# Kernel optimization log

Measured on AMD Instinct MI355X. Metric: run time of the kernel, lower is better.

The kernel has to match this reference:

```python
import jax, jax.numpy as jnp
import numpy as np

# SS2D (VMamba-style): CrossScan (4 directional traversals) -> per-direction
# input-dependent SSM params -> selective scan recurrence -> CrossMerge -> ChanLayerNorm.

B_SZ, D_IN, H_SZ, W_SZ = 8, 192, 64, 64   # d_inner = ssm_ratio * d_model = 2*96
N_ST, R_DT, K_GRP = 16, 6, 4               # d_state, dt_rank=ceil(96/16), 4 scan dirs
LN_EPS = 1e-5


def setup_inputs() -> dict:
    key = jax.random.key(0)
    ks = jax.random.split(key, 6)
    x = jax.random.normal(ks[0], (B_SZ, D_IN, H_SZ, W_SZ), dtype=jnp.float32)
    x_proj_weight = jax.random.normal(ks[1], (K_GRP, R_DT + 2 * N_ST, D_IN), dtype=jnp.float32) * 0.02
    dt_projs_weight = jax.random.normal(ks[2], (K_GRP, D_IN, R_DT), dtype=jnp.float32) * (R_DT ** -0.5)
    dt_projs_bias = jax.random.normal(ks[3], (K_GRP, D_IN), dtype=jnp.float32) * 0.1
    # A_log init: log(1..N) repeated per channel (mamba v0 init)
    A_logs = jnp.log(jnp.tile(jnp.arange(1, N_ST + 1, dtype=jnp.float32), (K_GRP * D_IN, 1)))
    Ds = jnp.ones((K_GRP * D_IN,), dtype=jnp.float32)
    ln_g = jnp.ones((1, D_IN, 1, 1), dtype=jnp.float32)
    ln_b = jnp.zeros((1, D_IN, 1, 1), dtype=jnp.float32)
    return dict(x=x, x_proj_weight=x_proj_weight, dt_projs_weight=dt_projs_weight,
                dt_projs_bias=dt_projs_bias, A_logs=A_logs, Ds=Ds, ln_g=ln_g, ln_b=ln_b)


def _ss2d(x, x_proj_weight, dt_projs_weight, dt_projs_bias, A_logs, Ds, ln_g, ln_b):
    B, D, H, W = x.shape
    L = H * W
    K = x_proj_weight.shape[0]
    N = A_logs.shape[1]
    R = dt_projs_weight.shape[2]

    # ---- CrossScan: 4 directional flattenings -> xs [B,K,D,L] ----
    x0 = x.reshape(B, D, L)                         # row-major
    x1 = x.transpose(0, 1, 3, 2).reshape(B, D, L)   # column-major (transpose H,W)
    xs = jnp.stack([x0, x1, x0[..., ::-1], x1[..., ::-1]], axis=1)

    # ---- input-dependent SSM params ----
    x_dbl = jnp.einsum('bkdl,kcd->bkcl', xs, x_proj_weight)      # [B,K,R+2N,L]
    dts, Bs, Cs = jnp.split(x_dbl, [R, R + N], axis=2)           # [B,K,R,L],[B,K,N,L],[B,K,N,L]
    dts = jnp.einsum('bkrl,kdr->bkdl', dts, dt_projs_weight)     # [B,K,D,L]
    A = -jnp.exp(A_logs.astype(jnp.float32)).reshape(K, D, N)    # [K,D,N]
    delta = jax.nn.softplus(dts + dt_projs_bias[None, :, :, None])  # [B,K,D,L]

    # ---- selective scan: h_t = exp(delta*A)*h_{t-1} + delta*B_t*u_t; y_t = C_t.h_t ----
    def step(h, inp):
        u_t, d_t, B_t, C_t = inp                     # [B,K,D],[B,K,D],[B,K,N],[B,K,N]
        h = jnp.exp(d_t[..., None] * A) * h + (d_t * u_t)[..., None] * B_t[:, :, None, :]
        y = jnp.einsum('bkdn,bkn->bkd', h, C_t)
        return h, y

    h0 = jnp.zeros((B, K, D, N), dtype=jnp.float32)
    seq = (xs.transpose(3, 0, 1, 2), delta.transpose(3, 0, 1, 2),
           Bs.transpose(3, 0, 1, 2), Cs.transpose(3, 0, 1, 2))
    _, ys = jax.lax.scan(step, h0, seq)              # [L,B,K,D]
    ys = ys.transpose(1, 2, 3, 0) + Ds.reshape(K, D)[None, :, :, None] * xs  # [B,K,D,L]

    # ---- CrossMerge: undo flips/transpose and sum the 4 directions ----
    ym = ys[:, 0:2] + ys[:, 2:4][..., ::-1]          # [B,2,D,L]
    y = ym[:, 0] + ym[:, 1].reshape(B, D, W, H).transpose(0, 1, 3, 2).reshape(B, D, L)
    y = y.reshape(B, D, H, W)

    # ---- ChanLayerNorm over channel dim (biased var) ----
    mean = jnp.mean(y, axis=1, keepdims=True)
    var = jnp.var(y, axis=1, keepdims=True)
    return (y - mean) / jnp.sqrt(var + LN_EPS) * ln_g + ln_b


def reference(x, x_proj_weight, dt_projs_weight, dt_projs_bias, A_logs, Ds, ln_g, ln_b):
    return _ss2d(x, x_proj_weight, dt_projs_weight, dt_projs_bias, A_logs, Ds, ln_g, ln_b)
```

## Files before the change

kernel.cpp:

```cpp
#include <hip/hip_runtime.h>
#include <cstdint>
#include <cstddef>


#define L2E 1.4426950408889634f
#define LN2 0.6931471805599453f
#define NCH 64
#define CHL 64

typedef float f32x2 __attribute__((ext_vector_type(2)));
typedef float f32x4 __attribute__((ext_vector_type(4)));

static __device__ __forceinline__ float fast_rcp(float x) {
#if defined(__has_builtin)
#if __has_builtin(__builtin_amdgcn_rcpf)
  return __builtin_amdgcn_rcpf(x);
#else
  return 1.f / x;
#endif
#else
  return 1.f / x;
#endif
}

static __device__ __forceinline__ f32x2 pk_mul_vv(f32x2 a, f32x2 b) {
  f32x2 d; asm("v_pk_mul_f32 %0, %1, %2" : "=v"(d) : "v"(a), "v"(b)); return d;
}
static __device__ __forceinline__ f32x2 pk_mul_bh(f32x2 a, f32x2 b) {
  f32x2 d;
  asm("v_pk_mul_f32 %0, %1, %2 op_sel:[0,1] op_sel_hi:[1,1]" : "=v"(d) : "v"(a), "v"(b));
  return d;
}
static __device__ __forceinline__ f32x2 pk_mul_sv(f32x2 s, f32x2 v) {
  f32x2 d; asm("v_pk_mul_f32 %0, %1, %2" : "=v"(d) : "s"(s), "v"(v)); return d;
}
static __device__ __forceinline__ f32x2 pk_mul_vs(f32x2 v, f32x2 s) {
  f32x2 d; asm("v_pk_mul_f32 %0, %1, %2" : "=v"(d) : "v"(v), "s"(s)); return d;
}
static __device__ __forceinline__ void pk_h(f32x2& h, f32x2 a, f32x2 t) {
  asm("v_pk_fma_f32 %0, %1, %0, %2" : "+v"(h) : "v"(a), "v"(t));
}
static __device__ __forceinline__ void pk_y(f32x2& y, f32x2 h, f32x2 cs) {
  asm("v_pk_fma_f32 %0, %1, %2, %0" : "+v"(y) : "v"(h), "s"(cs));
}

__global__ __launch_bounds__(256) void k0_xpose(const float* __restrict__ x,
                                                float* __restrict__ xP) {
  __shared__ float t[64 * 193];
  int b = blockIdx.x >> 6, p0 = (blockIdx.x & 63) << 6;
  for (int i = threadIdx.x; i < 64 * 192; i += 256) {
    int d = i >> 6, p = i & 63;
    t[p * 193 + d] = x[((size_t)(b * 192 + d)) * 4096 + p0 + p];
  }
  __syncthreads();
  float* dst = xP + ((size_t)b * 4096 + p0) * 192;
  for (int i = threadIdx.x; i < 64 * 192; i += 256) {
    int p = i / 192, d = i - p * 192;
    dst[i] = t[p * 193 + d];
  }
}

__global__ __launch_bounds__(256) void k1_proj(const float* __restrict__ x,
                                               const float* __restrict__ xpw,
                                               float* __restrict__ proj) {
  __shared__ float W[38 * 192];
  int bid = blockIdx.x;
  int t = bid & 15, k = (bid >> 4) & 3, b = bid >> 6;
  {
    const float4* src = (const float4*)(xpw + k * 38 * 192);
    float4* dst = (float4*)W;
    for (int i = threadIdx.x; i < 38 * 192 / 4; i += 256) dst[i] = src[i];
  }
  __syncthreads();

  int p = (t << 8) + threadIdx.x;
  const float* xb = x + (size_t)b * 192 * 4096 + p;
  float acc[38];
#pragma unroll
  for (int c = 0; c < 38; ++c) acc[c] = 0.f;

  for (int d0 = 0; d0 < 192; d0 += 8) {
    float xr[8];
#pragma unroll
    for (int j = 0; j < 8; ++j) xr[j] = xb[(size_t)(d0 + j) * 4096];
#pragma unroll
    for (int c = 0; c < 38; ++c) {
      const float* wr = &W[c * 192 + d0];
      float4 w0 = *(const float4*)wr;
      float4 w1 = *(const float4*)(wr + 4);
      float a0 = fmaf(w0.x, xr[0], fmaf(w0.y, xr[1], fmaf(w0.z, xr[2], w0.w * xr[3])));
      float a1 = fmaf(w1.x, xr[4], fmaf(w1.y, xr[5], fmaf(w1.z, xr[6], w1.w * xr[7])));
      acc[c] += a0 + a1;
    }
  }

  int hh = p >> 6, ww = p & 63;
  int lp = (k == 0) ? p
         : (k == 1) ? ((ww << 6) | hh)
         : (k == 2) ? (4095 - p)
                    : (4095 - ((ww << 6) | hh));
  float* row = proj + (((size_t)(b * 4 + k)) * 4096 + (size_t)lp) * 40;
#pragma unroll
  for (int q4 = 0; q4 < 9; ++q4) {
    float4 v; v.x = acc[q4 * 4]; v.y = acc[q4 * 4 + 1];
    v.z = acc[q4 * 4 + 2]; v.w = acc[q4 * 4 + 3];
    ((float4*)row)[q4] = v;
  }
  { float4 v; v.x = acc[36]; v.y = acc[37]; v.z = 0.f; v.w = 0.f; ((float4*)row)[9] = v; }
}

struct Pref { f32x4 b[10]; float u; };

static __device__ __forceinline__ void scan_step(const Pref& P, float bias,
                                                 const float w_[6], float Dk,
                                                 f32x2 h2[8], float& r, float* yp) {
  float dts = bias;
  dts = fmaf(w_[0], P.b[0].x, dts);
  dts = fmaf(w_[1], P.b[0].y, dts);
  dts = fmaf(w_[2], P.b[0].z, dts);
  dts = fmaf(w_[3], P.b[0].w, dts);
  dts = fmaf(w_[4], P.b[1].x, dts);
  dts = fmaf(w_[5], P.b[1].y, dts);
  float e1 = __builtin_exp2f(dts * L2E) + 1.f;
  float q = fast_rcp(e1);
  float delta = __builtin_log2f(e1) * LN2;
  float du = delta * P.u;
  r *= q;
  f32x2 a0; a0.x = q; a0.y = q * q;
  f32x2 a1 = pk_mul_bh(a0, a0);
  f32x2 a3 = pk_mul_bh(a1, a1);
  f32x2 a2 = pk_mul_bh(a0, a1);
  f32x2 a4 = pk_mul_bh(a0, a3);
  f32x2 a5 = pk_mul_bh(a1, a3);
  f32x2 a6 = pk_mul_bh(a2, a3);
  f32x2 a7 = pk_mul_bh(a3, a3);
  f32x2 du2; du2.x = du; du2.y = du;
  pk_h(h2[0], a0, pk_mul_sv(P.b[1].zw, du2));
  pk_h(h2[1], a1, pk_mul_sv(P.b[2].xy, du2));
  f32x2 ya = pk_mul_vs(h2[0], P.b[5].zw);
  f32x2 yb = pk_mul_vs(h2[1], P.b[6].xy);
  pk_h(h2[2], a2, pk_mul_sv(P.b[2].zw, du2));
  pk_y(ya, h2[2], P.b[6].zw);
  pk_h(h2[3], a3, pk_mul_sv(P.b[3].xy, du2));
  pk_y(yb, h2[3], P.b[7].xy);
  pk_h(h2[4], a4, pk_mul_sv(P.b[3].zw, du2));
  pk_y(ya, h2[4], P.b[7].zw);
  pk_h(h2[5], a5, pk_mul_sv(P.b[4].xy, du2));
  pk_y(yb, h2[5], P.b[8].xy);
  pk_h(h2[6], a6, pk_mul_sv(P.b[4].zw, du2));
  pk_y(ya, h2[6], P.b[8].zw);
  pk_h(h2[7], a7, pk_mul_sv(P.b[5].xy, du2));
  pk_y(yb, h2[7], P.b[9].xy);
  f32x2 yt = ya + yb;
  *yp = fmaf(Dk, P.u, yt.x + yt.y);
}

__global__ __launch_bounds__(192) void k2a_scan(const float* __restrict__ xP,
                                                const float* __restrict__ proj,
                                                const float* __restrict__ dtw,
                                                const float* __restrict__ dtb,
                                                const float* __restrict__ Ds,
                                                float* __restrict__ ys,
                                                float* __restrict__ hout,
                                                float* __restrict__ Rc) {
  int wg = blockIdx.x;
  int c = wg & (NCH - 1), bk = wg >> 6;
  int k = bk & 3, b = bk >> 2;
  int d = threadIdx.x;

  float w_[6];
  {
    const float* wrow = dtw + (size_t)(k * 192 + d) * 6;
#pragma unroll
    for (int r = 0; r < 6; ++r) w_[r] = wrow[r];
  }
  float bias = dtb[k * 192 + d];
  float Dk = (k == 0) ? (Ds[d] + Ds[192 + d] + Ds[384 + d] + Ds[576 + d]) : 0.f;

  int l0 = c * CHL;
  int p0s  = (k == 0) ? l0 : (k == 1) ? c : (k == 2) ? (4095 - l0) : (4095 - c);
  int pstr = (k == 0) ? 1  : (k == 1) ? 64 : (k == 2) ? -1 : -64;
  ptrdiff_t pinc = (ptrdiff_t)pstr * 192;

  const float* up = xP + ((size_t)b * 4096 + (size_t)p0s) * 192 + d;
  float* yp = ys + (((size_t)(k * 8 + b)) * 4096 + (size_t)p0s) * 192 + d;
  const float* pr = proj + ((size_t)bk * 4096 + l0) * 40;

  f32x2 h2[8];
#pragma unroll
  for (int j = 0; j < 8; ++j) { h2[j].x = 0.f; h2[j].y = 0.f; }
  float r = 1.f;

  Pref A, Bp;
#pragma unroll
  for (int i = 0; i < 10; ++i) A.b[i] = ((const f32x4*)pr)[i];
  A.u = *up;
  pr += 40; up += pinc;

  for (int t = 0; t < CHL - 2; t += 2) {
#pragma unroll
    for (int i = 0; i < 10; ++i) Bp.b[i] = ((const f32x4*)pr)[i];
    Bp.u = *up; pr += 40; up += pinc;
    scan_step(A, bias, w_, Dk, h2, r, yp); yp += pinc;
#pragma unroll
    for (int i = 0; i < 10; ++i) A.b[i] = ((const f32x4*)pr)[i];
    A.u = *up; pr += 40; up += pinc;
    scan_step(Bp, bias, w_, Dk, h2, r, yp); yp += pinc;
  }
#pragma unroll
  for (int i = 0; i < 10; ++i) Bp.b[i] = ((const f32x4*)pr)[i];
  Bp.u = *up;
  scan_step(A, bias, w_, Dk, h2, r, yp); yp += pinc;
  scan_step(Bp, bias, w_, Dk, h2, r, yp);

  float* hst = hout + (((size_t)bk * NCH + c) * 16) * 192 + d;
#pragma unroll
  for (int j = 0; j < 8; ++j) {
    hst[(size_t)(2 * j) * 192]     = h2[j].x;
    hst[(size_t)(2 * j + 1) * 192] = h2[j].y;
  }
  Rc[((size_t)bk * NCH + c) * 192 + d] = r;
}

__global__ __launch_bounds__(192) void k2b_pfx(float* __restrict__ hout,
                                               const float* __restrict__ Rc) {
  int bk = blockIdx.x >> 4, n = blockIdx.x & 15;
  int d = threadIdx.x;
  int e = n + 1;
  float H = 0.f;
  for (int c0 = 0; c0 < NCH; c0 += 4) {
    float hl[4], R[4];
#pragma unroll
    for (int j = 0; j < 4; ++j) {
      size_t cb = (size_t)bk * NCH + c0 + j;
      hl[j] = hout[(cb * 16 + n) * 192 + d];
      R[j] = Rc[cb * 192 + d];
    }
#pragma unroll
    for (int j = 0; j < 4; ++j) {
      size_t cb = (size_t)bk * NCH + c0 + j;
      hout[(cb * 16 + n) * 192 + d] = H;
      float R1 = R[j], R2 = R1 * R1, R4 = R2 * R2, R8 = R4 * R4;
      float Rp = 1.f;
      if (e & 1) Rp *= R1;
      if (e & 2) Rp *= R2;
      if (e & 4) Rp *= R4;
      if (e & 8) Rp *= R8;
      H = fmaf(Rp, H, hl[j]);
    }
  }
}

__global__ __launch_bounds__(192) void k2c_fix(const float* __restrict__ proj,
                                               const float* __restrict__ dtw,
                                               const float* __restrict__ dtb,
                                               const float* __restrict__ hout,
                                               float* __restrict__ ys) {
  int wg = blockIdx.x;
  int c = wg & (NCH - 1), bk = wg >> 6;
  if (c == 0) return;
  int k = bk & 3, b = bk >> 2;
  int d = threadIdx.x;

  float w_[6];
  {
    const float* wrow = dtw + (size_t)(k * 192 + d) * 6;
#pragma unroll
    for (int r = 0; r < 6; ++r) w_[r] = wrow[r];
  }
  float bias = dtb[k * 192 + d];

  f32x2 H2[8];
  {
    const float* hr = hout + (((size_t)bk * NCH + c) * 16) * 192 + d;
#pragma unroll
    for (int j = 0; j < 8; ++j) {
      H2[j].x = hr[(size_t)(2 * j) * 192];
      H2[j].y = hr[(size_t)(2 * j + 1) * 192];
    }
  }

  int l0 = c * CHL;
  int p0s  = (k == 0) ? l0 : (k == 1) ? c : (k == 2) ? (4095 - l0) : (4095 - c);
  int pstr = (k == 0) ? 1  : (k == 1) ? 64 : (k == 2) ? -1 : -64;
  ptrdiff_t pinc = (ptrdiff_t)pstr * 192;

  const float* pr = proj + ((size_t)bk * 4096 + l0) * 40;
  float* yp = ys + (((size_t)(k * 8 + b)) * 4096 + (size_t)p0s) * 192 + d;
  float r = 1.f;

  for (int t = 0; t < CHL; ++t) {
    f32x4 v0 = *(const f32x4*)pr;
    f32x2 v1 = *(const f32x2*)(pr + 4);
    f32x2 c0 = *(const f32x2*)(pr + 22);
    f32x2 c1 = *(const f32x2*)(pr + 24);
    f32x2 c2 = *(const f32x2*)(pr + 26);
    f32x2 c3 = *(const f32x2*)(pr + 28);
    f32x2 c4 = *(const f32x2*)(pr + 30);
    f32x2 c5 = *(const f32x2*)(pr + 32);
    f32x2 c6 = *(const f32x2*)(pr + 34);
    f32x2 c7 = *(const f32x2*)(pr + 36);

    float dts = bias;
    dts = fmaf(w_[0], v0.x, dts);
    dts = fmaf(w_[1], v0.y, dts);
    dts = fmaf(w_[2], v0.z, dts);
    dts = fmaf(w_[3], v0.w, dts);
    dts = fmaf(w_[4], v1.x, dts);
    dts = fmaf(w_[5], v1.y, dts);
    float e1 = __builtin_exp2f(dts * L2E) + 1.f;
    float q = fast_rcp(e1);
    r *= q;
    if (__all(r < 1e-8f)) break;
    f32x2 p0; p0.x = r; p0.y = r * r;
    f32x2 rp1 = pk_mul_bh(p0, p0);
    f32x2 rp3 = pk_mul_bh(rp1, rp1);
    f32x2 rp2 = pk_mul_bh(p0, rp1);
    f32x2 rp4 = pk_mul_bh(p0, rp3);
    f32x2 rp5 = pk_mul_bh(rp1, rp3);
    f32x2 rp6 = pk_mul_bh(rp2, rp3);
    f32x2 rp7 = pk_mul_bh(rp3, rp3);
    f32x2 ya = pk_mul_vs(pk_mul_vv(H2[0], p0),  c0);
    f32x2 yb = pk_mul_vs(pk_mul_vv(H2[1], rp1), c1);
    pk_y(ya, pk_mul_vv(H2[2], rp2), c2);
    pk_y(yb, pk_mul_vv(H2[3], rp3), c3);
    pk_y(ya, pk_mul_vv(H2[4], rp4), c4);
    pk_y(yb, pk_mul_vv(H2[5], rp5), c5);
    pk_y(ya, pk_mul_vv(H2[6], rp6), c6);
    pk_y(yb, pk_mul_vv(H2[7], rp7), c7);
    f32x2 yt = ya + yb;
    *yp += yt.x + yt.y;
    pr += 40; yp += pinc;
  }
}

__global__ __launch_bounds__(256) void k3_ln(const float* __restrict__ ys,
                                             const float* __restrict__ g,
                                             const float* __restrict__ bta,
                                             float* __restrict__ out) {
  __shared__ float tile[64 * 193];
  __shared__ float ps[4][64], pq[4][64];
  __shared__ float mstat[64], rstat[64];
  int b = blockIdx.x >> 6, p0 = (blockIdx.x & 63) << 6;
  const float* s0 = ys + ((size_t)(0 * 8 + b) * 4096 + p0) * 192;
  const float* s1 = ys + ((size_t)(1 * 8 + b) * 4096 + p0) * 192;
  const float* s2 = ys + ((size_t)(2 * 8 + b) * 4096 + p0) * 192;
  const float* s3 = ys + ((size_t)(3 * 8 + b) * 4096 + p0) * 192;
  for (int i = threadIdx.x; i < 64 * 192; i += 256) {
    int p = i / 192, dd = i - p * 192;
    tile[p * 193 + dd] = (s0[i] + s1[i]) + (s2[i] + s3[i]);
  }
  __syncthreads();
  {
    int p = threadIdx.x & 63, qd = threadIdx.x >> 6;
    float s = 0.f, s2a = 0.f;
#pragma unroll
    for (int j = 0; j < 48; ++j) {
      float v = tile[p * 193 + qd * 48 + j];
      s += v; s2a = fmaf(v, v, s2a);
    }
    ps[qd][p] = s; pq[qd][p] = s2a;
  }
  __syncthreads();
  if (threadIdx.x < 64) {
    int p = threadIdx.x;
    float S = ps[0][p] + ps[1][p] + ps[2][p] + ps[3][p];
    float Q = pq[0][p] + pq[1][p] + pq[2][p] + pq[3][p];
    float mu = S * (1.f / 192.f);
    float var = Q * (1.f / 192.f) - mu * mu;
    mstat[p] = mu;
    rstat[p] = rsqrtf(var + 1e-5f);
  }
  __syncthreads();
  for (int i = threadIdx.x; i < 64 * 192; i += 256) {
    int dd = i >> 6, p = i & 63;
    float v = (tile[p * 193 + dd] - mstat[p]) * rstat[p] * g[dd] + bta[dd];
    out[((size_t)(b * 192 + dd)) * 4096 + p0 + p] = v;
  }
}

extern "C" void kernel_launch(void* const* d_in, const int* in_sizes, int n_in,
                              void* d_out, int out_size, void* d_ws, size_t ws_size,
                              hipStream_t stream) {
  const float* x   = (const float*)d_in[0];
  const float* xpw = (const float*)d_in[1];
  const float* dtw = (const float*)d_in[2];
  const float* dtb = (const float*)d_in[3];
  const float* Ds  = (const float*)d_in[5];
  const float* g   = (const float*)d_in[6];
  const float* bta = (const float*)d_in[7];
  float* out = (float*)d_out;

  char* ws = (char*)d_ws;
  float* xP   = (float*)(ws);
  float* proj = (float*)(ws + 25165824);
  float* ys   = (float*)(ws + 46137344);
  float* hout = (float*)(ws + 146800640);
  float* Rc   = (float*)(ws + 171966464);

  k0_xpose<<<512, 256, 0, stream>>>(x, xP);
  k1_proj<<<512, 256, 0, stream>>>(x, xpw, proj);
  k2a_scan<<<2048, 192, 0, stream>>>(xP, proj, dtw, dtb, Ds, ys, hout, Rc);
  k2b_pfx<<<512, 192, 0, stream>>>(hout, Rc);
  k2c_fix<<<2048, 192, 0, stream>>>(proj, dtw, dtb, hout, ys);
  k3_ln<<<512, 256, 0, stream>>>(ys, g, bta, out);
}
```

Baseline: 200.7 us.

## Fuse transpose into projection kernel and loosen fix-up early-exit threshold

Drops the separate k0_xpose kernel. The k=0 blocks of k1_proj now write the channel-last copy xP from the values they already load, which saves one launch and one full read of x. The xP writes are 192-float strided per thread rather than coalesced. In k2c_fix the dt dot product is split into independent partial sums for more ILP, and the C coefficients move from SGPR operands to VGPR operands. The early-exit threshold on the decay product rises from 1e-8 to 2e-5, which skips more correction steps at some cost in accuracy.

```diff
diff --git a/kernel.cpp b/kernel.cpp
--- a/kernel.cpp
+++ b/kernel.cpp
@@ -43,26 +43,14 @@
 static __device__ __forceinline__ void pk_y(f32x2& y, f32x2 h, f32x2 cs) {
   asm("v_pk_fma_f32 %0, %1, %2, %0" : "+v"(y) : "v"(h), "s"(cs));
 }
-
-__global__ __launch_bounds__(256) void k0_xpose(const float* __restrict__ x,
-                                                float* __restrict__ xP) {
-  __shared__ float t[64 * 193];
-  int b = blockIdx.x >> 6, p0 = (blockIdx.x & 63) << 6;
-  for (int i = threadIdx.x; i < 64 * 192; i += 256) {
-    int d = i >> 6, p = i & 63;
-    t[p * 193 + d] = x[((size_t)(b * 192 + d)) * 4096 + p0 + p];
-  }
-  __syncthreads();
-  float* dst = xP + ((size_t)b * 4096 + p0) * 192;
-  for (int i = threadIdx.x; i < 64 * 192; i += 256) {
-    int p = i / 192, d = i - p * 192;
-    dst[i] = t[p * 193 + d];
-  }
+static __device__ __forceinline__ void pk_yv(f32x2& y, f32x2 h, f32x2 c) {
+  asm("v_pk_fma_f32 %0, %1, %2, %0" : "+v"(y) : "v"(h), "v"(c));
 }
 
 __global__ __launch_bounds__(256) void k1_proj(const float* __restrict__ x,
                                                const float* __restrict__ xpw,
-                                               float* __restrict__ proj) {
+                                               float* __restrict__ proj,
+                                               float* __restrict__ xP) {
   __shared__ float W[38 * 192];
   int bid = blockIdx.x;
   int t = bid & 15, k = (bid >> 4) & 3, b = bid >> 6;
@@ -75,6 +63,7 @@
 
   int p = (t << 8) + threadIdx.x;
   const float* xb = x + (size_t)b * 192 * 4096 + p;
+  float* xProw = xP + ((size_t)b * 4096 + (size_t)p) * 192;
   float acc[38];
 #pragma unroll
   for (int c = 0; c < 38; ++c) acc[c] = 0.f;
@@ -83,6 +72,12 @@
     float xr[8];
 #pragma unroll
     for (int j = 0; j < 8; ++j) xr[j] = xb[(size_t)(d0 + j) * 4096];
+    if (k == 0) {
+      float4 v0; v0.x = xr[0]; v0.y = xr[1]; v0.z = xr[2]; v0.w = xr[3];
+      float4 v1; v1.x = xr[4]; v1.y = xr[5]; v1.z = xr[6]; v1.w = xr[7];
+      *(float4*)(xProw + d0) = v0;
+      *(float4*)(xProw + d0 + 4) = v1;
+    }
 #pragma unroll
     for (int c = 0; c < 38; ++c) {
       const float* wr = &W[c * 192 + d0];
@@ -301,17 +296,14 @@
     f32x2 c6 = *(const f32x2*)(pr + 34);
     f32x2 c7 = *(const f32x2*)(pr + 36);
 
-    float dts = bias;
-    dts = fmaf(w_[0], v0.x, dts);
-    dts = fmaf(w_[1], v0.y, dts);
-    dts = fmaf(w_[2], v0.z, dts);
-    dts = fmaf(w_[3], v0.w, dts);
-    dts = fmaf(w_[4], v1.x, dts);
-    dts = fmaf(w_[5], v1.y, dts);
+    float m01 = fmaf(w_[1], v0.y, fmaf(w_[0], v0.x, bias));
+    float m23 = fmaf(w_[3], v0.w, w_[2] * v0.z);
+    float m45 = fmaf(w_[5], v1.y, w_[4] * v1.x);
+    float dts = (m01 + m23) + m45;
     float e1 = __builtin_exp2f(dts * L2E) + 1.f;
     float q = fast_rcp(e1);
     r *= q;
-    if (__all(r < 1e-8f)) break;
+    if (__all(r < 2e-5f)) break;
     f32x2 p0; p0.x = r; p0.y = r * r;
     f32x2 rp1 = pk_mul_bh(p0, p0);
     f32x2 rp3 = pk_mul_bh(rp1, rp1);
@@ -320,14 +312,14 @@
     f32x2 rp5 = pk_mul_bh(rp1, rp3);
     f32x2 rp6 = pk_mul_bh(rp2, rp3);
     f32x2 rp7 = pk_mul_bh(rp3, rp3);
-    f32x2 ya = pk_mul_vs(pk_mul_vv(H2[0], p0),  c0);
-    f32x2 yb = pk_mul_vs(pk_mul_vv(H2[1], rp1), c1);
-    pk_y(ya, pk_mul_vv(H2[2], rp2), c2);
-    pk_y(yb, pk_mul_vv(H2[3], rp3), c3);
-    pk_y(ya, pk_mul_vv(H2[4], rp4), c4);
-    pk_y(yb, pk_mul_vv(H2[5], rp5), c5);
-    pk_y(ya, pk_mul_vv(H2[6], rp6), c6);
-    pk_y(yb, pk_mul_vv(H2[7], rp7), c7);
+    f32x2 ya = pk_mul_vv(pk_mul_vv(H2[0], p0),  c0);
+    f32x2 yb = pk_mul_vv(pk_mul_vv(H2[1], rp1), c1);
+    pk_yv(ya, pk_mul_vv(H2[2], rp2), c2);
+    pk_yv(yb, pk_mul_vv(H2[3], rp3), c3);
+    pk_yv(ya, pk_mul_vv(H2[4], rp4), c4);
+    pk_yv(yb, pk_mul_vv(H2[5], rp5), c5);
+    pk_yv(ya, pk_mul_vv(H2[6], rp6), c6);
+    pk_yv(yb, pk_mul_vv(H2[7], rp7), c7);
     f32x2 yt = ya + yb;
     *yp += yt.x + yt.y;
     pr += 40; yp += pinc;
@@ -398,8 +390,7 @@
   float* hout = (float*)(ws + 146800640);
   float* Rc   = (float*)(ws + 171966464);
 
-  k0_xpose<<<512, 256, 0, stream>>>(x, xP);
-  k1_proj<<<512, 256, 0, stream>>>(x, xpw, proj);
+  k1_proj<<<512, 256, 0, stream>>>(x, xpw, proj, xP);
   k2a_scan<<<2048, 192, 0, stream>>>(xP, proj, dtw, dtb, Ds, ys, hout, Rc);
   k2b_pfx<<<512, 192, 0, stream>>>(hout, Rc);
   k2c_fix<<<2048, 192, 0, stream>>>(proj, dtw, dtb, hout, ys);
```

After: 181.1 us. 1.11x faster.
